# Kernel tuning notes

Hardware: AMD Instinct MI355X
Metric: run time of the kernel (lower is better)

## Reference

```python
import jax, jax.numpy as jnp
import numpy as np

N = 100000
E = 1600000
IN, HID, OUT = 128, 128, 64


def setup_inputs() -> dict:
    key = jax.random.key(0)
    k = jax.random.split(key, 8)
    x = jax.random.normal(k[0], (N, IN), dtype=jnp.float32)
    src = jax.random.randint(k[1], (E,), 0, N)
    dst = jax.random.randint(k[2], (E,), 0, N)
    # Glorot-ish init for the per-layer fc_neigh weights + biases
    W1 = jax.random.normal(k[3], (IN, HID), dtype=jnp.float32) / np.sqrt(IN)
    b1 = jnp.zeros((HID,), dtype=jnp.float32)
    W2 = jax.random.normal(k[4], (HID, OUT), dtype=jnp.float32) / np.sqrt(HID)
    b2 = jnp.zeros((OUT,), dtype=jnp.float32)
    return {"x": x, "src": src, "dst": dst, "W1": W1, "b1": b1, "W2": W2, "b2": b2}


def _sage_gcn_layer(h, src, dst, W, b):
    # DGL SAGEConv aggregator_type='gcn':
    #   neigh = sum_{u in N(v)} h_u ; h_neigh = (neigh + h_v) / (deg(v) + 1)
    #   out = h_neigh @ W + b   (fc_self unused for 'gcn')
    msg = h[src]                                              # [E, d] gather
    agg = jax.ops.segment_sum(msg, dst, num_segments=N)       # [N, d] scatter-add
    deg = jax.ops.segment_sum(jnp.ones((E,), h.dtype), dst, num_segments=N)
    h_neigh = (agg + h) / (deg[:, None] + 1.0)
    return h_neigh @ W + b


def reference(x, src, dst, W1, b1, W2, b2):
    # Dropout in eval mode (identity), as for a deterministic correctness baseline.
    h = _sage_gcn_layer(x, src, dst, W1, b1)
    h = jax.nn.relu(h)
    h = _sage_gcn_layer(h, src, dst, W2, b2)
    return h
```

## Files before the change

### kernel.cpp

```cpp
#include <hip/hip_runtime.h>

#define NN 100000
#define EE 1600000
#define FD 128
#define NBK 391
#define BCAP 5120
#define CHUNK 4096

typedef __attribute__((ext_vector_type(8))) short bf16x8;
typedef __attribute__((ext_vector_type(4))) float f32x4;

static __device__ __forceinline__ unsigned bfpack(float lo, float hi) {
  unsigned a = __float_as_uint(lo), b = __float_as_uint(hi);
  a = (a + 0x7FFFu + ((a >> 16) & 1u)) >> 16;
  b = (b + 0x7FFFu + ((b >> 16) & 1u)) >> 16;
  return a | (b << 16);
}
static __device__ __forceinline__ ushort bfround(float x) {
  unsigned u = __float_as_uint(x);
  u = (u + 0x7FFFu + ((u >> 16) & 1u)) >> 16;
  return (ushort)u;
}
static __device__ __forceinline__ float bflo(unsigned u) {
  return __uint_as_float(u << 16);
}
static __device__ __forceinline__ float bfhi(unsigned u) {
  return __uint_as_float(u & 0xFFFF0000u);
}

__global__ __launch_bounds__(256) void pass1_wconv(const int* __restrict__ src,
                                                   const int* __restrict__ dst,
                                                   unsigned* __restrict__ gcur,
                                                   unsigned* __restrict__ arena,
                                                   const float* __restrict__ W1,
                                                   const float* __restrict__ W2,
                                                   ushort* __restrict__ Wt1g,
                                                   ushort* __restrict__ Wt2g) {
  __shared__ unsigned hist[NBK + 1];
  __shared__ unsigned scan[512];
  __shared__ unsigned gpos[NBK + 1];
  __shared__ unsigned sorted[CHUNK];
  int t = threadIdx.x;

  if (blockIdx.x >= NBK) {
    int i = (int)(blockIdx.x - NBK) * 256 + t;
    if (i < 128 * 128) {
      int k = i >> 7, c = i & 127;
      Wt1g[c * 128 + k] = bfround(W1[i]);
    } else {
      int j = i - 128 * 128;
      if (j < 128 * 64) {
        int k = j >> 6, c = j & 63;
        Wt2g[c * 128 + k] = bfround(W2[j]);
      }
    }
    return;
  }

  int base = blockIdx.x * CHUNK;
  hist[t] = 0;
  if (t + 256 <= NBK) hist[t + 256] = 0;
  __syncthreads();

  int dreg[16], sreg[16];
#pragma unroll
  for (int j = 0; j < 16; ++j) {
    int e = base + t + j * 256;
    if (e < EE) {
      dreg[j] = dst[e];
      sreg[j] = src[e];
      atomicAdd(&hist[dreg[j] >> 8], 1u);
    } else {
      dreg[j] = -1;
      sreg[j] = 0;
    }
  }
  __syncthreads();

  scan[t] = (t < NBK) ? hist[t] : 0;
  scan[t + 256] = (t + 256 < NBK) ? hist[t + 256] : 0;
  __syncthreads();
  for (int d = 1; d < 512; d <<= 1) {
    unsigned r0 = (t >= d) ? scan[t - d] : 0;
    unsigned r1 = ((t + 256) >= d) ? scan[t + 256 - d] : 0;
    __syncthreads();
    scan[t] += r0;
    scan[t + 256] += r1;
    __syncthreads();
  }
  unsigned c0 = (t < NBK) ? scan[t] - hist[t] : 0;
  unsigned c1 = (t + 256 < NBK) ? scan[t + 256] - hist[t + 256] : 0;
  __syncthreads();
  if (t < NBK) hist[t] = c0;
  if (t + 256 < NBK) hist[t + 256] = c1;
  __syncthreads();

#pragma unroll
  for (int j = 0; j < 16; ++j) {
    if (dreg[j] >= 0) {
      int b = dreg[j] >> 8;
      unsigned pos = atomicAdd(&hist[b], 1u);
      sorted[pos] = ((unsigned)(dreg[j] & 255) << 20) | (unsigned)sreg[j];
    }
  }
  __syncthreads();

  if (t < NBK) {
    unsigned lo = t ? scan[t - 1] : 0;
    unsigned cntb = scan[t] - lo;
    if (cntb) gpos[t] = atomicAdd(&gcur[t], cntb);
  }
  if (t + 256 < NBK) {
    unsigned lo = scan[t + 255];
    unsigned cntb = scan[t + 256] - lo;
    if (cntb) gpos[t + 256] = atomicAdd(&gcur[t + 256], cntb);
  }
  __syncthreads();

  int w = t >> 6, lane = t & 63;
  for (int b = w; b < NBK; b += 4) {
    unsigned lo = b ? scan[b - 1] : 0;
    unsigned cntb = scan[b] - lo;
    if (!cntb) continue;
    unsigned gp = gpos[b];
    if (gp >= BCAP) continue;
    unsigned lim = min(gp + cntb, (unsigned)BCAP) - gp;
    for (unsigned i = lane; i < lim; i += 64)
      arena[(size_t)b * BCAP + gp + i] = sorted[lo + i];
  }
}

template <int NCOLS>
static __device__ __forceinline__ void gemm_body_f32(const float* __restrict__ A,
                                                     const ushort* __restrict__ Wtg,
                                                     ushort* __restrict__ out, int bid,
                                                     int t, ushort* Wt, ushort* As) {
  constexpr int NCT = NCOLS / 16;
  int node0 = bid * 64;
  for (int idx = t; idx < NCOLS * 16; idx += 256) {
    int flat = idx * 8;
    int c = flat >> 7, k = flat & 127;
    uint4 v = *reinterpret_cast<const uint4*>(Wtg + flat);
    *reinterpret_cast<uint4*>(&Wt[c * 136 + k]) = v;
  }
  {
    int r = t >> 2, cq = (t & 3) * 32;
    int row = node0 + r;
    if (row >= NN) row = NN - 1;
    const float4* s = reinterpret_cast<const float4*>(A + (size_t)row * FD + cq);
    unsigned dv[16];
#pragma unroll
    for (int q = 0; q < 8; ++q) {
      float4 f = s[q];
      dv[q * 2 + 0] = bfpack(f.x, f.y);
      dv[q * 2 + 1] = bfpack(f.z, f.w);
    }
    uint4* d = reinterpret_cast<uint4*>(&As[r * 136 + cq]);
#pragma unroll
    for (int q = 0; q < 4; ++q)
      d[q] = make_uint4(dv[q * 4 + 0], dv[q * 4 + 1], dv[q * 4 + 2], dv[q * 4 + 3]);
  }
  __syncthreads();

  int w = t >> 6, l = t & 63;
  int lr = l & 15, lq = l >> 4;
  f32x4 acc[NCT];
#pragma unroll
  for (int ct = 0; ct < NCT; ++ct) acc[ct] = (f32x4)0.0f;
  const ushort* aBase = &As[(w * 16 + lr) * 136 + lq * 8];
  const ushort* bBase = &Wt[lr * 136 + lq * 8];
#pragma unroll
  for (int ks = 0; ks < 4; ++ks) {
    bf16x8 a = *reinterpret_cast<const bf16x8*>(aBase + ks * 32);
#pragma unroll
    for (int ct = 0; ct < NCT; ++ct) {
      bf16x8 b = *reinterpret_cast<const bf16x8*>(bBase + ct * 16 * 136 + ks * 32);
      acc[ct] = __builtin_amdgcn_mfma_f32_16x16x32_bf16(a, b, acc[ct], 0, 0, 0);
    }
  }
  int rowb = node0 + w * 16 + lq * 4;
#pragma unroll
  for (int ct = 0; ct < NCT; ++ct) {
#pragma unroll
    for (int r = 0; r < 4; ++r) {
      int row = rowb + r;
      if (row < NN) out[(size_t)row * NCOLS + ct * 16 + lr] = bfround(acc[ct][r]);
    }
  }
}

__global__ __launch_bounds__(256) void pass2_gemm1(const unsigned* __restrict__ arena,
                                                   const unsigned* __restrict__ gcur,
                                                   int* __restrict__ nbr,
                                                   int* __restrict__ cur,
                                                   const float* __restrict__ x,
                                                   const ushort* __restrict__ Wt1g,
                                                   ushort* __restrict__ y1) {
  __shared__ __align__(16) char smem[52224];
  int t = threadIdx.x;

  if (blockIdx.x >= NBK) {
    gemm_body_f32<128>(x, Wt1g, y1, (int)(blockIdx.x - NBK), t, (ushort*)smem,
                       (ushort*)(smem + 34816));
    return;
  }

  unsigned* sh = (unsigned*)smem;
  unsigned* hist = sh + 512;
  unsigned* scn = hist + 256;
  unsigned* sorted = scn + 256;
  int b = blockIdx.x;

  unsigned v0 = (t < NBK) ? gcur[t] : 0;
  unsigned v1 = (t + 256 < NBK) ? gcur[t + 256] : 0;
  sh[t] = v0;
  sh[t + 256] = v1;
  __syncthreads();
  for (int d = 1; d < 512; d <<= 1) {
    unsigned r0 = (t >= d) ? sh[t - d] : 0;
    unsigned r1 = ((t + 256) >= d) ? sh[t + 256 - d] : 0;
    __syncthreads();
    sh[t] += r0;
    sh[t + 256] += r1;
    __syncthreads();
  }
  unsigned base = b ? sh[b - 1] : 0;
  unsigned cnt = min(sh[b] - base, (unsigned)BCAP);
  const unsigned* run = arena + (size_t)b * BCAP;

  hist[t] = 0;
  __syncthreads();
  for (unsigned i = t; i < cnt; i += 256) atomicAdd(&hist[run[i] >> 20], 1u);
  __syncthreads();
  scn[t] = hist[t];
  __syncthreads();
  for (int d = 1; d < 256; d <<= 1) {
    unsigned r = (t >= d) ? scn[t - d] : 0;
    __syncthreads();
    scn[t] += r;
    __syncthreads();
  }
  unsigned excl = scn[t] - hist[t];
  __syncthreads();
  hist[t] = excl;
  __syncthreads();
  for (unsigned i = t; i < cnt; i += 256) {
    unsigned v = run[i];
    unsigned pos = atomicAdd(&hist[v >> 20], 1u);
    sorted[pos] = v & 0xFFFFFu;
  }
  __syncthreads();
  for (unsigned i = t; i < cnt; i += 256) nbr[base + i] = (int)sorted[i];
  int node = b * 256 + t;
  if (node < NN) cur[node] = (int)(base + scn[t]);
}

static __device__ __forceinline__ uint2 gather_pair(const unsigned* __restrict__ Y,
                                                    const int* __restrict__ cur,
                                                    const int* __restrict__ nbr, int v0,
                                                    int lane, float2 bv) {
  int v1 = v0 + 1;
  int e0a = __builtin_amdgcn_readfirstlane(v0 ? cur[v0 - 1] : 0);
  int e1a = __builtin_amdgcn_readfirstlane(cur[v0]);
  int e1b = __builtin_amdgcn_readfirstlane(cur[v1]);
  int e0b = e1a;
  float invA = 1.0f / (float)(e1a - e0a + 1);
  float invB = 1.0f / (float)(e1b - e0b + 1);

  float ax0 = 0.f, ay0 = 0.f, ax1 = 0.f, ay1 = 0.f;
  int ja = e0a, jb = e0b;
  while (ja + 4 <= e1a && jb + 4 <= e1b) {
    unsigned a0 = Y[(size_t)nbr[ja + 0] * 64 + lane];
    unsigned a1 = Y[(size_t)nbr[ja + 1] * 64 + lane];
    unsigned a2 = Y[(size_t)nbr[ja + 2] * 64 + lane];
    unsigned a3 = Y[(size_t)nbr[ja + 3] * 64 + lane];
    unsigned b0 = Y[(size_t)nbr[jb + 0] * 64 + lane];
    unsigned b1 = Y[(size_t)nbr[jb + 1] * 64 + lane];
    unsigned b2 = Y[(size_t)nbr[jb + 2] * 64 + lane];
    unsigned b3 = Y[(size_t)nbr[jb + 3] * 64 + lane];
    ax0 += (bflo(a0) + bflo(a1)) + (bflo(a2) + bflo(a3));
    ay0 += (bfhi(a0) + bfhi(a1)) + (bfhi(a2) + bfhi(a3));
    ax1 += (bflo(b0) + bflo(b1)) + (bflo(b2) + bflo(b3));
    ay1 += (bfhi(b0) + bfhi(b1)) + (bfhi(b2) + bfhi(b3));
    ja += 4;
    jb += 4;
  }
  for (; ja + 4 <= e1a; ja += 4) {
    unsigned a0 = Y[(size_t)nbr[ja + 0] * 64 + lane];
    unsigned a1 = Y[(size_t)nbr[ja + 1] * 64 + lane];
    unsigned a2 = Y[(size_t)nbr[ja + 2] * 64 + lane];
    unsigned a3 = Y[(size_t)nbr[ja + 3] * 64 + lane];
    ax0 += (bflo(a0) + bflo(a1)) + (bflo(a2) + bflo(a3));
    ay0 += (bfhi(a0) + bfhi(a1)) + (bfhi(a2) + bfhi(a3));
  }
  for (; jb + 4 <= e1b; jb += 4) {
    unsigned b0 = Y[(size_t)nbr[jb + 0] * 64 + lane];
    unsigned b1 = Y[(size_t)nbr[jb + 1] * 64 + lane];
    unsigned b2 = Y[(size_t)nbr[jb + 2] * 64 + lane];
    unsigned b3 = Y[(size_t)nbr[jb + 3] * 64 + lane];
    ax1 += (bflo(b0) + bflo(b1)) + (bflo(b2) + bflo(b3));
    ay1 += (bfhi(b0) + bfhi(b1)) + (bfhi(b2) + bfhi(b3));
  }
  for (; ja < e1a; ++ja) {
    unsigned a = Y[(size_t)nbr[ja] * 64 + lane];
    ax0 += bflo(a);
    ay0 += bfhi(a);
  }
  for (; jb < e1b; ++jb) {
    unsigned b = Y[(size_t)nbr[jb] * 64 + lane];
    ax1 += bflo(b);
    ay1 += bfhi(b);
  }
  unsigned sv0 = Y[(size_t)v0 * 64 + lane];
  unsigned sv1 = Y[(size_t)v1 * 64 + lane];
  float rx0 = fmaxf((ax0 + bflo(sv0)) * invA + bv.x, 0.f);
  float ry0 = fmaxf((ay0 + bfhi(sv0)) * invA + bv.y, 0.f);
  float rx1 = fmaxf((ax1 + bflo(sv1)) * invB + bv.x, 0.f);
  float ry1 = fmaxf((ay1 + bfhi(sv1)) * invB + bv.y, 0.f);
  uint2 r;
  r.x = bfpack(rx0, ry0);
  r.y = bfpack(rx1, ry1);
  return r;
}

__global__ __launch_bounds__(256) void layer2_fused(const unsigned* __restrict__ Y,
                                                    const int* __restrict__ cur,
                                                    const int* __restrict__ nbr,
                                                    const float* __restrict__ b1,
                                                    const ushort* __restrict__ Wt2g,
                                                    ushort* __restrict__ y2) {
  __shared__ ushort Wt[64 * 136];
  __shared__ ushort As[64 * 136];
  int t = threadIdx.x;
  int node0 = blockIdx.x * 64;
  int w = t >> 6, lane = t & 63;

  for (int idx = t; idx < 64 * 16; idx += 256) {
    int flat = idx * 8;
    int c = flat >> 7, k = flat & 127;
    uint4 v = *reinterpret_cast<const uint4*>(Wt2g + flat);
    *reinterpret_cast<uint4*>(&Wt[c * 136 + k]) = v;
  }

  float2 bv = reinterpret_cast<const float2*>(b1)[lane];
  for (int p = 0; p < 16; p += 2) {
    int r = w * 16 + p;
    int v0 = node0 + r;
    if (v0 >= NN) {
      *reinterpret_cast<unsigned*>(&As[r * 136 + 2 * lane]) = 0;
      *reinterpret_cast<unsigned*>(&As[(r + 1) * 136 + 2 * lane]) = 0;
      continue;
    }
    uint2 h = gather_pair(Y, cur, nbr, v0, lane, bv);
    *reinterpret_cast<unsigned*>(&As[r * 136 + 2 * lane]) = h.x;
    *reinterpret_cast<unsigned*>(&As[(r + 1) * 136 + 2 * lane]) = h.y;
  }
  __syncthreads();

  int lr = lane & 15, lq = lane >> 4;
  f32x4 acc[4];
#pragma unroll
  for (int ct = 0; ct < 4; ++ct) acc[ct] = (f32x4)0.0f;
  const ushort* aBase = &As[(w * 16 + lr) * 136 + lq * 8];
  const ushort* bBase = &Wt[lr * 136 + lq * 8];
#pragma unroll
  for (int ks = 0; ks < 4; ++ks) {
    bf16x8 a = *reinterpret_cast<const bf16x8*>(aBase + ks * 32);
#pragma unroll
    for (int ct = 0; ct < 4; ++ct) {
      bf16x8 b = *reinterpret_cast<const bf16x8*>(bBase + ct * 16 * 136 + ks * 32);
      acc[ct] = __builtin_amdgcn_mfma_f32_16x16x32_bf16(a, b, acc[ct], 0, 0, 0);
    }
  }
  int rowb = node0 + w * 16 + lq * 4;
#pragma unroll
  for (int ct = 0; ct < 4; ++ct) {
#pragma unroll
    for (int r = 0; r < 4; ++r) {
      int row = rowb + r;
      if (row < NN) y2[(size_t)row * 64 + ct * 16 + lr] = bfround(acc[ct][r]);
    }
  }
}

__global__ __launch_bounds__(256) void gather64_kernel(const ushort* __restrict__ Y,
                                                       const int* __restrict__ cur,
                                                       const int* __restrict__ nbr,
                                                       const float* __restrict__ bias,
                                                       float* __restrict__ out) {
  int wv = (blockIdx.x * 256 + threadIdx.x) >> 6;
  int v0 = wv * 2;
  if (v0 >= NN) return;
  int v1 = v0 + 1;
  int lane = threadIdx.x & 63;
  int e0a = __builtin_amdgcn_readfirstlane(v0 ? cur[v0 - 1] : 0);
  int e1a = __builtin_amdgcn_readfirstlane(cur[v0]);
  int e1b = __builtin_amdgcn_readfirstlane(cur[v1]);
  int e0b = e1a;
  float invA = 1.0f / (float)(e1a - e0a + 1);
  float invB = 1.0f / (float)(e1b - e0b + 1);

  float s0 = 0.f, s1 = 0.f;
  int ja = e0a, jb = e0b;
  while (ja + 4 <= e1a && jb + 4 <= e1b) {
    float a0 = __uint_as_float((unsigned)Y[(size_t)nbr[ja + 0] * 64 + lane] << 16);
    float a1 = __uint_as_float((unsigned)Y[(size_t)nbr[ja + 1] * 64 + lane] << 16);
    float a2 = __uint_as_float((unsigned)Y[(size_t)nbr[ja + 2] * 64 + lane] << 16);
    float a3 = __uint_as_float((unsigned)Y[(size_t)nbr[ja + 3] * 64 + lane] << 16);
    float b0 = __uint_as_float((unsigned)Y[(size_t)nbr[jb + 0] * 64 + lane] << 16);
    float b1 = __uint_as_float((unsigned)Y[(size_t)nbr[jb + 1] * 64 + lane] << 16);
    float b2 = __uint_as_float((unsigned)Y[(size_t)nbr[jb + 2] * 64 + lane] << 16);
    float b3 = __uint_as_float((unsigned)Y[(size_t)nbr[jb + 3] * 64 + lane] << 16);
    s0 += (a0 + a1) + (a2 + a3);
    s1 += (b0 + b1) + (b2 + b3);
    ja += 4;
    jb += 4;
  }
  for (; ja + 4 <= e1a; ja += 4) {
    float a0 = __uint_as_float((unsigned)Y[(size_t)nbr[ja + 0] * 64 + lane] << 16);
    float a1 = __uint_as_float((unsigned)Y[(size_t)nbr[ja + 1] * 64 + lane] << 16);
    float a2 = __uint_as_float((unsigned)Y[(size_t)nbr[ja + 2] * 64 + lane] << 16);
    float a3 = __uint_as_float((unsigned)Y[(size_t)nbr[ja + 3] * 64 + lane] << 16);
    s0 += (a0 + a1) + (a2 + a3);
  }
  for (; jb + 4 <= e1b; jb += 4) {
    float b0 = __uint_as_float((unsigned)Y[(size_t)nbr[jb + 0] * 64 + lane] << 16);
    float b1 = __uint_as_float((unsigned)Y[(size_t)nbr[jb + 1] * 64 + lane] << 16);
    float b2 = __uint_as_float((unsigned)Y[(size_t)nbr[jb + 2] * 64 + lane] << 16);
    float b3 = __uint_as_float((unsigned)Y[(size_t)nbr[jb + 3] * 64 + lane] << 16);
    s1 += (b0 + b1) + (b2 + b3);
  }
  for (; ja < e1a; ++ja)
    s0 += __uint_as_float((unsigned)Y[(size_t)nbr[ja] * 64 + lane] << 16);
  for (; jb < e1b; ++jb)
    s1 += __uint_as_float((unsigned)Y[(size_t)nbr[jb] * 64 + lane] << 16);

  float self0 = __uint_as_float((unsigned)Y[(size_t)v0 * 64 + lane] << 16);
  float self1 = __uint_as_float((unsigned)Y[(size_t)v1 * 64 + lane] << 16);
  float bvv = bias[lane];
  out[(size_t)v0 * 64 + lane] = (s0 + self0) * invA + bvv;
  out[(size_t)v1 * 64 + lane] = (s1 + self1) * invB + bvv;
}

extern "C" void kernel_launch(void* const* d_in, const int* in_sizes, int n_in,
                              void* d_out, int out_size, void* d_ws, size_t ws_size,
                              hipStream_t stream) {
  const float* x  = (const float*)d_in[0];
  const int* src  = (const int*)d_in[1];
  const int* dst  = (const int*)d_in[2];
  const float* W1 = (const float*)d_in[3];
  const float* b1 = (const float*)d_in[4];
  const float* W2 = (const float*)d_in[5];
  const float* b2 = (const float*)d_in[6];
  float* out = (float*)d_out;

  char* ws = (char*)d_ws;
  ushort*   Wt1g  = (ushort*)(ws + 0);
  ushort*   Wt2g  = (ushort*)(ws + 32768);
  unsigned* gcur  = (unsigned*)(ws + 49152);
  int*      cur   = (int*)(ws + 53248);
  int*      nbr   = (int*)(ws + 453248);
  unsigned* arena = (unsigned*)(ws + 6853248);
  ushort*   y1    = (ushort*)(ws + 14860928);
  ushort*   y2    = (ushort*)(ws + 40460928);

  const int gemmBlocks = (NN + 63) / 64;
  const int gathBlocks = (NN / 2 + 3) / 4;

  hipMemsetAsync(gcur, 0, NBK * sizeof(unsigned), stream);
  pass1_wconv<<<NBK + 96, 256, 0, stream>>>(src, dst, gcur, arena, W1, W2, Wt1g, Wt2g);
  pass2_gemm1<<<NBK + gemmBlocks, 256, 0, stream>>>(arena, gcur, nbr, cur, x, Wt1g, y1);
  layer2_fused<<<gemmBlocks, 256, 0, stream>>>((const unsigned*)y1, cur, nbr, b1, Wt2g, y2);
  gather64_kernel<<<gathBlocks, 256, 0, stream>>>(y2, cur, nbr, b2, out);
}
```

Baseline: 198.6 us.

## Split fused layer-2 gather+GEMM into separate gather and MFMA GEMM kernels

```diff
diff --git a/kernel.cpp b/kernel.cpp
--- a/kernel.cpp
+++ b/kernel.cpp
@@ -255,11 +255,67 @@
   if (node < NN) cur[node] = (int)(base + scn[t]);
 }
 
-static __device__ __forceinline__ uint2 gather_pair(const unsigned* __restrict__ Y,
-                                                    const int* __restrict__ cur,
-                                                    const int* __restrict__ nbr, int v0,
-                                                    int lane, float2 bv) {
+__global__ __launch_bounds__(256) void mfma_gemm64(const ushort* __restrict__ A,
+                                                   const ushort* __restrict__ Wtg,
+                                                   ushort* __restrict__ out) {
+  __shared__ ushort Wt[64 * 136];
+  __shared__ ushort As[64 * 136];
+  int t = threadIdx.x;
+  int node0 = blockIdx.x * 64;
+
+  for (int idx = t; idx < 64 * 16; idx += 256) {
+    int flat = idx * 8;
+    int c = flat >> 7, k = flat & 127;
+    uint4 v = *reinterpret_cast<const uint4*>(Wtg + flat);
+    *reinterpret_cast<uint4*>(&Wt[c * 136 + k]) = v;
+  }
+  {
+    int r = t >> 2, cq = (t & 3) * 32;
+    int row = node0 + r;
+    if (row >= NN) row = NN - 1;
+    const uint4* s = reinterpret_cast<const uint4*>(A + (size_t)row * FD + cq);
+    uint4* d = reinterpret_cast<uint4*>(&As[r * 136 + cq]);
+    d[0] = s[0]; d[1] = s[1]; d[2] = s[2]; d[3] = s[3];
+  }
+  __syncthreads();
+
+  int w = t >> 6, l = t & 63;
+  int lr = l & 15, lq = l >> 4;
+  f32x4 acc[4];
+#pragma unroll
+  for (int ct = 0; ct < 4; ++ct) acc[ct] = (f32x4)0.0f;
+  const ushort* aBase = &As[(w * 16 + lr) * 136 + lq * 8];
+  const ushort* bBase = &Wt[lr * 136 + lq * 8];
+#pragma unroll
+  for (int ks = 0; ks < 4; ++ks) {
+    bf16x8 a = *reinterpret_cast<const bf16x8*>(aBase + ks * 32);
+#pragma unroll
+    for (int ct = 0; ct < 4; ++ct) {
+      bf16x8 b = *reinterpret_cast<const bf16x8*>(bBase + ct * 16 * 136 + ks * 32);
+      acc[ct] = __builtin_amdgcn_mfma_f32_16x16x32_bf16(a, b, acc[ct], 0, 0, 0);
+    }
+  }
+  int rowb = node0 + w * 16 + lq * 4;
+#pragma unroll
+  for (int ct = 0; ct < 4; ++ct) {
+#pragma unroll
+    for (int r = 0; r < 4; ++r) {
+      int row = rowb + r;
+      if (row < NN) out[(size_t)row * 64 + ct * 16 + lr] = bfround(acc[ct][r]);
+    }
+  }
+}
+
+__global__ __launch_bounds__(256) void gather128_kernel(const unsigned* __restrict__ Y,
+                                                        const int* __restrict__ cur,
+                                                        const int* __restrict__ nbr,
+                                                        const float* __restrict__ bias,
+                                                        unsigned* __restrict__ outp) {
+  int wv = (blockIdx.x * 256 + threadIdx.x) >> 6;
+  int v0 = wv * 2;
+  if (v0 >= NN) return;
   int v1 = v0 + 1;
+  int lane = threadIdx.x & 63;
   int e0a = __builtin_amdgcn_readfirstlane(v0 ? cur[v0 - 1] : 0);
   int e1a = __builtin_amdgcn_readfirstlane(cur[v0]);
   int e1b = __builtin_amdgcn_readfirstlane(cur[v1]);
@@ -313,74 +369,13 @@
   }
   unsigned sv0 = Y[(size_t)v0 * 64 + lane];
   unsigned sv1 = Y[(size_t)v1 * 64 + lane];
+  float2 bv = reinterpret_cast<const float2*>(bias)[lane];
   float rx0 = fmaxf((ax0 + bflo(sv0)) * invA + bv.x, 0.f);
   float ry0 = fmaxf((ay0 + bfhi(sv0)) * invA + bv.y, 0.f);
   float rx1 = fmaxf((ax1 + bflo(sv1)) * invB + bv.x, 0.f);
   float ry1 = fmaxf((ay1 + bfhi(sv1)) * invB + bv.y, 0.f);
-  uint2 r;
-  r.x = bfpack(rx0, ry0);
-  r.y = bfpack(rx1, ry1);
-  return r;
-}
-
-__global__ __launch_bounds__(256) void layer2_fused(const unsigned* __restrict__ Y,
-                                                    const int* __restrict__ cur,
-                                                    const int* __restrict__ nbr,
-                                                    const float* __restrict__ b1,
-                                                    const ushort* __restrict__ Wt2g,
-                                                    ushort* __restrict__ y2) {
-  __shared__ ushort Wt[64 * 136];
-  __shared__ ushort As[64 * 136];
-  int t = threadIdx.x;
-  int node0 = blockIdx.x * 64;
-  int w = t >> 6, lane = t & 63;
-
-  for (int idx = t; idx < 64 * 16; idx += 256) {
-    int flat = idx * 8;
-    int c = flat >> 7, k = flat & 127;
-    uint4 v = *reinterpret_cast<const uint4*>(Wt2g + flat);
-    *reinterpret_cast<uint4*>(&Wt[c * 136 + k]) = v;
-  }
-
-  float2 bv = reinterpret_cast<const float2*>(b1)[lane];
-  for (int p = 0; p < 16; p += 2) {
-    int r = w * 16 + p;
-    int v0 = node0 + r;
-    if (v0 >= NN) {
-      *reinterpret_cast<unsigned*>(&As[r * 136 + 2 * lane]) = 0;
-      *reinterpret_cast<unsigned*>(&As[(r + 1) * 136 + 2 * lane]) = 0;
-      continue;
-    }
-    uint2 h = gather_pair(Y, cur, nbr, v0, lane, bv);
-    *reinterpret_cast<unsigned*>(&As[r * 136 + 2 * lane]) = h.x;
-    *reinterpret_cast<unsigned*>(&As[(r + 1) * 136 + 2 * lane]) = h.y;
-  }
-  __syncthreads();
-
-  int lr = lane & 15, lq = lane >> 4;
-  f32x4 acc[4];
-#pragma unroll
-  for (int ct = 0; ct < 4; ++ct) acc[ct] = (f32x4)0.0f;
-  const ushort* aBase = &As[(w * 16 + lr) * 136 + lq * 8];
-  const ushort* bBase = &Wt[lr * 136 + lq * 8];
-#pragma unroll
-  for (int ks = 0; ks < 4; ++ks) {
-    bf16x8 a = *reinterpret_cast<const bf16x8*>(aBase + ks * 32);
-#pragma unroll
-    for (int ct = 0; ct < 4; ++ct) {
-      bf16x8 b = *reinterpret_cast<const bf16x8*>(bBase + ct * 16 * 136 + ks * 32);
-      acc[ct] = __builtin_amdgcn_mfma_f32_16x16x32_bf16(a, b, acc[ct], 0, 0, 0);
-    }
-  }
-  int rowb = node0 + w * 16 + lq * 4;
-#pragma unroll
-  for (int ct = 0; ct < 4; ++ct) {
-#pragma unroll
-    for (int r = 0; r < 4; ++r) {
-      int row = rowb + r;
-      if (row < NN) y2[(size_t)row * 64 + ct * 16 + lr] = bfround(acc[ct][r]);
-    }
-  }
+  outp[(size_t)v0 * 64 + lane] = bfpack(rx0, ry0);
+  outp[(size_t)v1 * 64 + lane] = bfpack(rx1, ry1);
 }
 
 __global__ __launch_bounds__(256) void gather64_kernel(const ushort* __restrict__ Y,
@@ -462,7 +457,8 @@
   int*      nbr   = (int*)(ws + 453248);
   unsigned* arena = (unsigned*)(ws + 6853248);
   ushort*   y1    = (ushort*)(ws + 14860928);
-  ushort*   y2    = (ushort*)(ws + 40460928);
+  ushort*   h1    = (ushort*)(ws + 40460928);
+  ushort*   y2    = (ushort*)(ws + 66060928);
 
   const int gemmBlocks = (NN + 63) / 64;
   const int gathBlocks = (NN / 2 + 3) / 4;
@@ -470,6 +466,8 @@
   hipMemsetAsync(gcur, 0, NBK * sizeof(unsigned), stream);
   pass1_wconv<<<NBK + 96, 256, 0, stream>>>(src, dst, gcur, arena, W1, W2, Wt1g, Wt2g);
   pass2_gemm1<<<NBK + gemmBlocks, 256, 0, stream>>>(arena, gcur, nbr, cur, x, Wt1g, y1);
-  layer2_fused<<<gemmBlocks, 256, 0, stream>>>((const unsigned*)y1, cur, nbr, b1, Wt2g, y2);
+  gather128_kernel<<<gathBlocks, 256, 0, stream>>>((const unsigned*)y1, cur, nbr, b1,
+                                                   (unsigned*)h1);
+  mfma_gemm64<<<gemmBlocks, 256, 0, stream>>>(h1, Wt2g, y2);
   gather64_kernel<<<gathBlocks, 256, 0, stream>>>(y2, cur, nbr, b2, out);
 }
```

Measured after the change: 184.9 us. 6.9% less time.
